# Kernel tuning notes

Measured on AMD Instinct MI355X. Metric: run time of the kernel, lower is better.

The kernel has to match this reference:

```python
import jax, jax.numpy as jnp
import numpy as np

GRID_LENGTH = 8.0
GRID_SIZE = 32
ATOM_TYPE = 6


def generate_grid(grid_length, grid_size):
    # matches torch generate_grid: x varies slowest, z fastest -> meshgrid 'ij'
    half = grid_length / 2.0
    ticks = jnp.linspace(-half, half, grid_size, dtype=jnp.float32)
    gx, gy, gz = jnp.meshgrid(ticks, ticks, ticks, indexing='ij')
    return jnp.stack([gx, gy, gz], axis=-1)  # (G,G,G,3)


def setup_inputs() -> dict:
    key = jax.random.key(0)
    k1, k2 = jax.random.split(key)
    distance_vector = jax.random.normal(k1, (4, 32, 16, 3), dtype=jnp.float32) * 2.0
    atomic_numbers = jax.random.randint(k2, (32, 16), 0, 10, dtype=jnp.int64 if jax.config.read('jax_enable_x64') else jnp.int32)
    sigma = jnp.ones((1,), dtype=jnp.float32)
    return {"distance_vector": distance_vector, "atomic_numbers": atomic_numbers, "sigma": sigma}


def reference(distance_vector, atomic_numbers, sigma):
    # distance_vector: (B, A, N, 3); atomic_numbers: (A, N); sigma: (1,)
    grid = generate_grid(GRID_LENGTH, GRID_SIZE)  # (G,G,G,3)
    # diff: (B, A, N, G, G, G, 3)
    diff = grid[None, None, None] - distance_vector[:, :, :, None, None, None, :]
    sq = jnp.sum(diff * diff, axis=-1)  # ||grid - dv||^2, (B,A,N,G,G,G)
    coeff = -0.5 / (sigma[0] * sigma[0])
    box = jnp.exp(coeff * sq)
    mask = (atomic_numbers == ATOM_TYPE).astype(box.dtype)  # (A,N)
    # masked sum over neighbor axis N -> (B, A, G, G, G)
    out = jnp.sum(box * mask[None, :, :, None, None, None], axis=2)
    return out
```

## Files before the change

kernel.cpp:

```cpp
#include <hip/hip_runtime.h>
#include <hip/hip_bf16.h>

#define G 32
#define NNBR 16
#define ATOM_TYPE 6

__global__ __launch_bounds__(256) void voxel_kernel(
    const float* __restrict__ dv,
    const int*   __restrict__ an,
    const float* __restrict__ sigma,
    float*       __restrict__ out)
{
    const int ba    = blockIdx.x;
    const int a     = ba & 31;
    const int islab = blockIdx.y;
    const int tid   = threadIdx.x;

    __shared__ float sEx[NNBR][G];
    __shared__ float sEy[NNBR][G];
    __shared__ float sEz[NNBR][G];
    __shared__ int   sIdx[NNBR];
    __shared__ int   sM;

    if (tid == 0) {
        int m = 0;
        #pragma unroll
        for (int n = 0; n < NNBR; ++n) {
            if (an[a * NNBR + n] == ATOM_TYPE) sIdx[m++] = n;
        }
        sM = m;
    }
    __syncthreads();

    const int   M     = sM;
    const float s     = sigma[0];
    const float coeff = -0.5f / (s * s);
    const float step  = 8.0f / 31.0f;

    for (int idx = tid; idx < M * G; idx += 256) {
        const int m = idx >> 5;
        const int i = idx & 31;
        const int n = sIdx[m];
        const float* d = dv + ((size_t)ba * NNBR + n) * 3;
        const float t  = -4.0f + (float)i * step;
        const float dx = t - d[0];
        const float dy = t - d[1];
        const float dz = t - d[2];
        sEx[m][i] = __expf(coeff * dx * dx);
        sEy[m][i] = __expf(coeff * dy * dy);
        sEz[m][i] = __expf(coeff * dz * dz);
    }
    __syncthreads();

    const int k = tid & 31;
    float ez[NNBR];
    for (int m = 0; m < M; ++m) ez[m] = sEz[m][k];

    float* outp = out + (size_t)ba * (G * G * G) + (size_t)islab * 4096;

    #pragma unroll
    for (int sstep = 0; sstep < 16; ++sstep) {
        const int vl = tid + (sstep << 8);
        const int j  = (vl >> 5) & 31;
        const int il = vl >> 10;
        const int i  = islab * 4 + il;
        float acc = 0.0f;
        for (int m = 0; m < M; ++m) {
            acc += sEx[m][i] * (sEy[m][j] * ez[m]);
        }
        outp[vl] = acc;
    }
}

extern "C" void kernel_launch(void* const* d_in, const int* in_sizes, int n_in,
                              void* d_out, int out_size, void* d_ws, size_t ws_size,
                              hipStream_t stream) {
    const float* dv    = (const float*)d_in[0];
    const int*   an    = (const int*)d_in[1];
    const float* sigma = (const float*)d_in[2];
    float*       out   = (float*)d_out;

    dim3 grid(4 * 32, 8);
    dim3 block(256);
    voxel_kernel<<<grid, block, 0, stream>>>(dv, an, sigma, out);
}
```

Before: 67.45 us.

## Register-tile 4x4 outputs per thread with float4 stores and ballot-based mask compaction

Each thread now computes a 4(i) x 4(k) block of outputs at a fixed j, reading Ex and Ez as float4 from shared memory and reusing them across 16 accumulators. Output is written with vectorized float4 stores instead of scalar ones. The serial single-thread neighbor compaction is replaced by a wavefront ballot and popcount, and neighbor coordinates are staged in shared memory. This cuts LDS traffic, removes the dynamically indexed ez register array, and widens stores, at the cost of more accumulator registers.

```diff
diff --git a/kernel.cpp b/kernel.cpp
--- a/kernel.cpp
+++ b/kernel.cpp
@@ -16,20 +16,23 @@
     const int islab = blockIdx.y;
     const int tid   = threadIdx.x;
 
-    __shared__ float sEx[NNBR][G];
-    __shared__ float sEy[NNBR][G];
-    __shared__ float sEz[NNBR][G];
+    __shared__ __align__(16) float sEx[NNBR][G];
+    __shared__ __align__(16) float sEy[NNBR][G];
+    __shared__ __align__(16) float sEz[NNBR][G];
+    __shared__ float sDv[NNBR * 3];
     __shared__ int   sIdx[NNBR];
     __shared__ int   sM;
 
-    if (tid == 0) {
-        int m = 0;
-        #pragma unroll
-        for (int n = 0; n < NNBR; ++n) {
-            if (an[a * NNBR + n] == ATOM_TYPE) sIdx[m++] = n;
-        }
-        sM = m;
+    if (tid < NNBR * 3) sDv[tid] = dv[(size_t)ba * (NNBR * 3) + tid];
+
+    int flag = 0;
+    if (tid < NNBR) flag = (an[a * NNBR + tid] == ATOM_TYPE) ? 1 : 0;
+    unsigned long long mask = __ballot(flag);
+    if (flag) {
+        int pos = __popcll(mask & ((1ull << tid) - 1ull));
+        sIdx[pos] = tid;
     }
+    if (tid == 0) sM = (int)__popcll(mask);
     __syncthreads();
 
     const int   M     = sM;
@@ -41,35 +44,39 @@
         const int m = idx >> 5;
         const int i = idx & 31;
         const int n = sIdx[m];
-        const float* d = dv + ((size_t)ba * NNBR + n) * 3;
         const float t  = -4.0f + (float)i * step;
-        const float dx = t - d[0];
-        const float dy = t - d[1];
-        const float dz = t - d[2];
+        const float dx = t - sDv[3 * n + 0];
+        const float dy = t - sDv[3 * n + 1];
+        const float dz = t - sDv[3 * n + 2];
         sEx[m][i] = __expf(coeff * dx * dx);
         sEy[m][i] = __expf(coeff * dy * dy);
         sEz[m][i] = __expf(coeff * dz * dz);
     }
     __syncthreads();
 
-    const int k = tid & 31;
-    float ez[NNBR];
-    for (int m = 0; m < M; ++m) ez[m] = sEz[m][k];
+    const int j  = tid >> 3;
+    const int k0 = (tid & 7) * 4;
+    const int i0 = islab * 4;
 
-    float* outp = out + (size_t)ba * (G * G * G) + (size_t)islab * 4096;
+    float4 acc0 = {0.f, 0.f, 0.f, 0.f};
+    float4 acc1 = acc0, acc2 = acc0, acc3 = acc0;
 
-    #pragma unroll
-    for (int sstep = 0; sstep < 16; ++sstep) {
-        const int vl = tid + (sstep << 8);
-        const int j  = (vl >> 5) & 31;
-        const int il = vl >> 10;
-        const int i  = islab * 4 + il;
-        float acc = 0.0f;
-        for (int m = 0; m < M; ++m) {
-            acc += sEx[m][i] * (sEy[m][j] * ez[m]);
-        }
-        outp[vl] = acc;
+    for (int m = 0; m < M; ++m) {
+        const float  ey = sEy[m][j];
+        const float4 ez = *(const float4*)&sEz[m][k0];
+        const float4 ex = *(const float4*)&sEx[m][i0];
+        const float p0 = ex.x * ey, p1 = ex.y * ey, p2 = ex.z * ey, p3 = ex.w * ey;
+        acc0.x += p0 * ez.x; acc0.y += p0 * ez.y; acc0.z += p0 * ez.z; acc0.w += p0 * ez.w;
+        acc1.x += p1 * ez.x; acc1.y += p1 * ez.y; acc1.z += p1 * ez.z; acc1.w += p1 * ez.w;
+        acc2.x += p2 * ez.x; acc2.y += p2 * ez.y; acc2.z += p2 * ez.z; acc2.w += p2 * ez.w;
+        acc3.x += p3 * ez.x; acc3.y += p3 * ez.y; acc3.z += p3 * ez.z; acc3.w += p3 * ez.w;
     }
+
+    float4* out4 = (float4*)(out + (size_t)ba * (G * G * G) + (size_t)islab * 4096);
+    out4[0 * 256 + tid] = acc0;
+    out4[1 * 256 + tid] = acc1;
+    out4[2 * 256 + tid] = acc2;
+    out4[3 * 256 + tid] = acc3;
 }
 
 extern "C" void kernel_launch(void* const* d_in, const int* in_sizes, int n_in,
```

New measurement: 63.80 us. 1.06x faster.
